# Optimization experiments

Measured on AMD Instinct MI355X. Metric: run time of the kernel, lower is better.

## Reference

```python
import jax, jax.numpy as jnp
import numpy as np

NEG_INF = -1e20


def setup_inputs() -> dict:
    key = jax.random.key(0)
    kq, kk, kv, kl = jax.random.split(key, 4)
    B, NQ, NKV, D_QK, D_V = 16, 2048, 2048, 64, 64
    Q_batch = jax.random.normal(kq, (B, NQ, D_QK), dtype=jnp.float32)
    K_batch = jax.random.normal(kk, (B, NKV, D_QK), dtype=jnp.float32)
    V_batch = jax.random.normal(kv, (B, NKV, D_V), dtype=jnp.float32)
    valid_lens = jax.random.randint(kl, (B,), 0, NKV, dtype=jnp.int32)
    return {"Q_batch": Q_batch, "K_batch": K_batch, "V_batch": V_batch,
            "valid_lens": valid_lens}


def reference(Q_batch, K_batch, V_batch, valid_lens):
    d = Q_batch.shape[-1]
    # scores: (B, n_q, n_kv)
    S = jnp.einsum("bqd,bkd->bqk", Q_batch, K_batch) / jnp.sqrt(
        jnp.asarray(d, dtype=Q_batch.dtype))
    n_kv = S.shape[-1]
    # mask kv positions k >= valid_lens[b] (1-D valid_lens broadcast over queries)
    kv_idx = jnp.arange(n_kv)  # (n_kv,)
    mask = kv_idx[None, None, :] < valid_lens[:, None, None]  # (B,1,n_kv)
    S = jnp.where(mask, S, NEG_INF)
    W = jax.nn.softmax(S, axis=-1)
    # dropout rate is 0.0 (eval) -> identity
    return jnp.einsum("bqk,bkv->bqv", W, V_batch)
```

## Files before the change

### kernel.cpp

```cpp
#include <hip/hip_runtime.h>
#include <hip/hip_bf16.h>


typedef __attribute__((ext_vector_type(8))) short short8;
typedef __attribute__((ext_vector_type(4))) float float4v;
typedef __attribute__((ext_vector_type(16))) float f32x16;

#define BATCH 16
#define NQ 2048
#define NKV 2048
#define DH 64
#define KVB 64
#define NTILES (NKV / KVB)
#define TILE_ELEMS (KVB * DH)
#define NEG_INF -1e20f
#define SCALE_LOG2 0.180336880111120f

__device__ __forceinline__ short f2bf(float x) {
    union { float f; unsigned u; } v; v.f = x;
    unsigned r = (v.u + 0x7fffu + ((v.u >> 16) & 1u)) >> 16;
    return (short)r;
}

__device__ __forceinline__ short8 cvt8(float4v a, float4v b) {
    short8 r;
    r[0] = f2bf(a[0]); r[1] = f2bf(a[1]); r[2] = f2bf(a[2]); r[3] = f2bf(a[3]);
    r[4] = f2bf(b[0]); r[5] = f2bf(b[1]); r[6] = f2bf(b[2]); r[7] = f2bf(b[3]);
    return r;
}

__global__ __launch_bounds__(256) void prep_kernel(
    const float* __restrict__ K, const float* __restrict__ V,
    const int* __restrict__ valid_lens,
    short* __restrict__ Kf, short* __restrict__ Vf)
{
    const int b    = blockIdx.x >> 5;
    const int tile = blockIdx.x & 31;
    const int vlen = valid_lens[b];
    const int nkv  = (vlen == 0) ? NKV : vlen;
    if (tile * KVB >= nkv) return;

    const int tid = threadIdx.x;
    const int ln  = tid & 63;
    const int l31 = ln & 31;
    const int hi8 = (ln >> 5) * 8;
    const size_t gbase = ((size_t)b * NKV + (size_t)tile * KVB) * DH;
    short* kt = Kf + (((size_t)b * NTILES + tile) * TILE_ELEMS);
    short* vt = Vf + (((size_t)b * NTILES + tile) * TILE_ELEMS);

#pragma unroll
    for (int s = 0; s < 2; ++s) {
        const int kk = tid >> 6;
        const int kv = s * 32 + l31;
        const int d  = kk * 16 + hi8;
        const float* p = K + gbase + (size_t)kv * DH + d;
        *reinterpret_cast<short8*>(kt + (s * 256 + tid) * 8) =
            cvt8(*reinterpret_cast<const float4v*>(p),
                 *reinterpret_cast<const float4v*>(p + 4));
    }
#pragma unroll
    for (int t = 0; t < 2; ++t) {
        const int ks  = tid >> 6;
        const int d   = t * 32 + l31;
        const int kv0 = ks * 16 + hi8;
        short8 w;
#pragma unroll
        for (int j = 0; j < 8; ++j)
            w[j] = f2bf(V[gbase + (size_t)(kv0 + j) * DH + d]);
        *reinterpret_cast<short8*>(vt + (t * 256 + tid) * 8) = w;
    }
}

__global__ __launch_bounds__(512) void attn_fwd_kernel(
    const float* __restrict__ Q,
    const short* __restrict__ Kf,
    const short* __restrict__ Vf,
    const int* __restrict__ valid_lens,
    float* __restrict__ O)
{
    __shared__ float  mrg[4][2048];
    __shared__ float2 mlb[4][32];

    const int tid  = threadIdx.x;
    const int wave = tid >> 6;
    const int lane = tid & 63;
    const int l31  = lane & 31;
    const int hi   = lane >> 5;
    const int h    = wave >> 2;
    const int qsub = wave & 3;

    const int b  = blockIdx.x & 15;
    const int qt = blockIdx.x >> 4;
    const int qbase = qt * 128 + qsub * 32;

    const int vlen  = valid_lens[b];
    const int nkv   = (vlen == 0) ? NKV : vlen;
    const int tiles = (nkv + KVB - 1) / KVB;
    const int nh = (tiles + 1 - h) >> 1;

    const float* Qb = Q + ((size_t)b * NQ + qbase + l31) * DH;
    short8 qfrag[4];
#pragma unroll
    for (int kk = 0; kk < 4; ++kk) {
        const float* p = Qb + kk * 16 + hi * 8;
        float4v a = *reinterpret_cast<const float4v*>(p);
        float4v c = *reinterpret_cast<const float4v*>(p + 4);
#pragma unroll
        for (int j = 0; j < 4; ++j) { a[j] *= SCALE_LOG2; c[j] *= SCALE_LOG2; }
        qfrag[kk] = cvt8(a, c);
    }

    const short* Kfb = Kf + (size_t)b * NTILES * TILE_ELEMS + lane * 8;
    const short* Vfb = Vf + (size_t)b * NTILES * TILE_ELEMS + lane * 8;

    auto load_k = [&](short8 (&kf)[8], int tile) {
        const short* p = Kfb + (size_t)tile * TILE_ELEMS;
#pragma unroll
        for (int i = 0; i < 8; ++i)
            kf[i] = *reinterpret_cast<const short8*>(p + i * 512);
    };
    auto load_v = [&](short8 (&vf)[8], int tile) {
        const short* p = Vfb + (size_t)tile * TILE_ELEMS;
#pragma unroll
        for (int i = 0; i < 8; ++i)
            vf[i] = *reinterpret_cast<const short8*>(p + i * 512);
    };

    f32x16 acc_o[2];
#pragma unroll
    for (int t = 0; t < 2; ++t)
#pragma unroll
        for (int r = 0; r < 16; ++r) acc_o[t][r] = 0.f;
    float m = -INFINITY, lsum = 0.f;

    short8 kf0[8], kf1[8], vfr[8];

    auto body = [&](short8 (&kc)[8], short8 (&kn)[8], int it) {
        const int tile = 2 * it + h;
        load_v(vfr, tile);

        f32x16 acs[2];
#pragma unroll
        for (int s = 0; s < 2; ++s)
#pragma unroll
            for (int r = 0; r < 16; ++r) acs[s][r] = 0.f;
        __builtin_amdgcn_s_setprio(1);
#pragma unroll
        for (int s = 0; s < 2; ++s)
#pragma unroll
            for (int kk = 0; kk < 4; ++kk)
                acs[s] = __builtin_amdgcn_mfma_f32_32x32x16_bf16(
                    kc[s * 4 + kk], qfrag[kk], acs[s], 0, 0, 0);
        __builtin_amdgcn_s_setprio(0);

        if (it + 1 < nh) load_k(kn, 2 * (it + 1) + h);

        const int kvb0 = tile * KVB + 4 * hi;
#pragma unroll
        for (int s = 0; s < 2; ++s) {
            const int vlim = vlen - (kvb0 + s * 32);
#pragma unroll
            for (int r = 0; r < 16; ++r) {
                const int rc = (r & 3) + 8 * (r >> 2);
                acs[s][r] = (rc < vlim) ? acs[s][r] : NEG_INF;
            }
        }

        float mx[8];
#pragma unroll
        for (int r = 0; r < 8; ++r)
            mx[r] = fmaxf(fmaxf(acs[0][r], acs[0][r + 8]),
                          fmaxf(acs[1][r], acs[1][r + 8]));
#pragma unroll
        for (int d = 4; d; d >>= 1)
#pragma unroll
            for (int r = 0; r < d; ++r) mx[r] = fmaxf(mx[r], mx[r + d]);
        float x = mx[0];
        x = fmaxf(x, __shfl_xor(x, 32, 64));

        float mn = m;
        if (!__all(x <= m + 8.f)) {
            mn = fmaxf(m, x);
            const float alpha = exp2f(m - mn);
            m = mn;
            lsum *= alpha;
#pragma unroll
            for (int r = 0; r < 16; ++r) {
                const int rc = (r & 3) + 8 * (r >> 2);
                const float ar = __shfl(alpha, rc + 4 * hi, 64);
                acc_o[0][r] *= ar;
                acc_o[1][r] *= ar;
            }
        }

#pragma unroll
        for (int s = 0; s < 2; ++s)
#pragma unroll
            for (int r = 0; r < 16; ++r) acs[s][r] = exp2f(acs[s][r] - mn);
        float sm[8];
#pragma unroll
        for (int r = 0; r < 8; ++r)
            sm[r] = (acs[0][r] + acs[0][r + 8]) + (acs[1][r] + acs[1][r + 8]);
#pragma unroll
        for (int d = 4; d; d >>= 1)
#pragma unroll
            for (int r = 0; r < d; ++r) sm[r] += sm[r + d];
        float rs = sm[0];
        rs += __shfl_xor(rs, 32, 64);
        lsum += rs;

        unsigned pk[2][4][2];
#pragma unroll
        for (int s = 0; s < 2; ++s)
#pragma unroll
            for (int be = 0; be < 4; ++be)
#pragma unroll
                for (int c = 0; c < 2; ++c)
                    asm("v_cvt_pk_bf16_f32 %0, %1, %2"
                        : "=v"(pk[s][be][c])
                        : "v"(acs[s][4 * be + 2 * c]),
                          "v"(acs[s][4 * be + 2 * c + 1]));

        __builtin_amdgcn_s_setprio(1);
#pragma unroll
        for (int ks = 0; ks < 4; ++ks) {
            const int s = ks >> 1, g = ks & 1;
            unsigned w0 = pk[s][2 * g][0], w2 = pk[s][2 * g + 1][0];
            unsigned w1 = pk[s][2 * g][1], w3 = pk[s][2 * g + 1][1];
            asm("v_permlane32_swap_b32 %0, %1" : "+v"(w0), "+v"(w2));
            asm("v_permlane32_swap_b32 %0, %1" : "+v"(w1), "+v"(w3));
            union { unsigned u[4]; short8 s8; } pf;
            pf.u[0] = w0; pf.u[1] = w1; pf.u[2] = w2; pf.u[3] = w3;
#pragma unroll
            for (int t = 0; t < 2; ++t)
                acc_o[t] = __builtin_amdgcn_mfma_f32_32x32x16_bf16(
                    pf.s8, vfr[t * 4 + ks], acc_o[t], 0, 0, 0);
        }
        __builtin_amdgcn_s_setprio(0);
    };

    if (nh > 0) load_k(kf0, h);
    int it = 0;
    for (; it + 1 < nh; it += 2) {
        body(kf0, kf1, it);
        body(kf1, kf0, it + 1);
    }
    if (it < nh) body(kf0, kf1, it);

    if (h == 1) {
#pragma unroll
        for (int t = 0; t < 2; ++t)
#pragma unroll
            for (int r = 0; r < 16; ++r)
                mrg[qsub][(t * 16 + r) * 64 + lane] = acc_o[t][r];
        if (lane < 32) mlb[qsub][lane] = float2{m, lsum};
    }
    __syncthreads();
    if (h == 0) {
        const float2 o1 = mlb[qsub][l31];
        const float m1 = o1.x, l1 = o1.y;
        const float M  = (l1 > 0.f) ? fmaxf(m, m1) : m;
        const float w0 = exp2f(m - M);
        const float w1 = (l1 > 0.f) ? exp2f(m1 - M) : 0.f;
        const float L  = lsum * w0 + l1 * w1;
        const float a0 = w0 / L, a1 = w1 / L;
        float* Ob = O + ((size_t)b * NQ + qbase) * DH;
#pragma unroll
        for (int r = 0; r < 16; ++r) {
            const int rc = (r & 3) + 8 * (r >> 2);
            const float a0r = __shfl(a0, rc + 4 * hi, 64);
            const float a1r = __shfl(a1, rc + 4 * hi, 64);
#pragma unroll
            for (int t = 0; t < 2; ++t) {
                const float oh = mrg[qsub][(t * 16 + r) * 64 + lane];
                Ob[(size_t)(rc + 4 * hi) * DH + t * 32 + l31] =
                    acc_o[t][r] * a0r + oh * a1r;
            }
        }
    }
}

extern "C" void kernel_launch(void* const* d_in, const int* in_sizes, int n_in,
                              void* d_out, int out_size, void* d_ws, size_t ws_size,
                              hipStream_t stream) {
    const float* Q = (const float*)d_in[0];
    const float* K = (const float*)d_in[1];
    const float* V = (const float*)d_in[2];
    const int* vl  = (const int*)d_in[3];
    float* Out     = (float*)d_out;

    short* Kws = (short*)d_ws;
    short* Vws = Kws + (size_t)BATCH * NTILES * TILE_ELEMS;

    prep_kernel<<<dim3(BATCH * NTILES), dim3(256), 0, stream>>>(K, V, vl, Kws, Vws);
    attn_fwd_kernel<<<dim3(BATCH * (NQ / 128)), dim3(512), 0, stream>>>(
        Q, Kws, Vws, vl, Out);
}
```

Before: 43.85 us.

## Split KV range four ways per query tile and coalesce V prep transpose

The attention kernel now handles 64 queries per block, with four waves splitting the KV tiles for each 32-query group instead of two. This doubles the grid and gives each wave fewer serial tiles, which matters because valid lengths vary. Partial results from all four waves are merged through padded shared memory into coalesced float4 output stores. The prep kernel now reads V with vectorized row loads before transposing to bf16 fragments, replacing strided scalar loads. Masking is skipped on tiles that are fully valid. The trade-off is more merge work, more shared memory, and Q being loaded and converted for twice as many blocks.

```diff
diff --git a/kernel.cpp b/kernel.cpp
--- a/kernel.cpp
+++ b/kernel.cpp
@@ -3,6 +3,7 @@
 
 
 typedef __attribute__((ext_vector_type(8))) short short8;
+typedef __attribute__((ext_vector_type(4))) short short4v;
 typedef __attribute__((ext_vector_type(4))) float float4v;
 typedef __attribute__((ext_vector_type(16))) float f32x16;
 
@@ -58,16 +59,27 @@
             cvt8(*reinterpret_cast<const float4v*>(p),
                  *reinterpret_cast<const float4v*>(p + 4));
     }
-#pragma unroll
-    for (int t = 0; t < 2; ++t) {
-        const int ks  = tid >> 6;
-        const int d   = t * 32 + l31;
-        const int kv0 = ks * 16 + hi8;
-        short8 w;
-#pragma unroll
-        for (int j = 0; j < 8; ++j)
-            w[j] = f2bf(V[gbase + (size_t)(kv0 + j) * DH + d]);
-        *reinterpret_cast<short8*>(vt + (t * 256 + tid) * 8) = w;
+    {
+        const int kv0 = (tid >> 4) << 2;
+        const int d0  = (tid & 15) << 2;
+        const float* p = V + gbase + (size_t)kv0 * DH + d0;
+        float4v r0 = *reinterpret_cast<const float4v*>(p);
+        float4v r1 = *reinterpret_cast<const float4v*>(p + DH);
+        float4v r2 = *reinterpret_cast<const float4v*>(p + 2 * DH);
+        float4v r3 = *reinterpret_cast<const float4v*>(p + 3 * DH);
+        const int ks  = kv0 >> 4;
+        const int hiv = (kv0 >> 3) & 1;
+        const int j0  = kv0 & 7;
+#pragma unroll
+        for (int k = 0; k < 4; ++k) {
+            const int d    = d0 + k;
+            const int lanev = (d & 31) + 32 * hiv;
+            short4v w;
+            w[0] = f2bf(r0[k]); w[1] = f2bf(r1[k]);
+            w[2] = f2bf(r2[k]); w[3] = f2bf(r3[k]);
+            *reinterpret_cast<short4v*>(
+                vt + (((d >> 5) * 4 + ks) * 64 + lanev) * 8 + j0) = w;
+        }
     }
 }
 
@@ -78,25 +90,25 @@
     const int* __restrict__ valid_lens,
     float* __restrict__ O)
 {
-    __shared__ float  mrg[4][2048];
-    __shared__ float2 mlb[4][32];
+    __shared__ float  mrg[2][4][32][68];
+    __shared__ float2 mlb[2][4][32];
 
     const int tid  = threadIdx.x;
     const int wave = tid >> 6;
     const int lane = tid & 63;
     const int l31  = lane & 31;
     const int hi   = lane >> 5;
-    const int h    = wave >> 2;
-    const int qsub = wave & 3;
+    const int qsub = wave >> 2;
+    const int kvq  = wave & 3;
 
     const int b  = blockIdx.x & 15;
     const int qt = blockIdx.x >> 4;
-    const int qbase = qt * 128 + qsub * 32;
+    const int qbase = qt * 64 + qsub * 32;
 
     const int vlen  = valid_lens[b];
     const int nkv   = (vlen == 0) ? NKV : vlen;
     const int tiles = (nkv + KVB - 1) / KVB;
-    const int nh = (tiles + 1 - h) >> 1;
+    const int nh    = (tiles - kvq + 3) >> 2;
 
     const float* Qb = Q + ((size_t)b * NQ + qbase + l31) * DH;
     short8 qfrag[4];
@@ -136,7 +148,7 @@
     short8 kf0[8], kf1[8], vfr[8];
 
     auto body = [&](short8 (&kc)[8], short8 (&kn)[8], int it) {
-        const int tile = 2 * it + h;
+        const int tile = 4 * it + kvq;
         load_v(vfr, tile);
 
         f32x16 acs[2];
@@ -153,16 +165,18 @@
                     kc[s * 4 + kk], qfrag[kk], acs[s], 0, 0, 0);
         __builtin_amdgcn_s_setprio(0);
 
-        if (it + 1 < nh) load_k(kn, 2 * (it + 1) + h);
-
-        const int kvb0 = tile * KVB + 4 * hi;
-#pragma unroll
-        for (int s = 0; s < 2; ++s) {
-            const int vlim = vlen - (kvb0 + s * 32);
-#pragma unroll
-            for (int r = 0; r < 16; ++r) {
-                const int rc = (r & 3) + 8 * (r >> 2);
-                acs[s][r] = (rc < vlim) ? acs[s][r] : NEG_INF;
+        if (it + 1 < nh) load_k(kn, 4 * (it + 1) + kvq);
+
+        if (vlen < (tile + 1) * KVB) {
+            const int kvb0 = tile * KVB + 4 * hi;
+#pragma unroll
+            for (int s = 0; s < 2; ++s) {
+                const int vlim = vlen - (kvb0 + s * 32);
+#pragma unroll
+                for (int r = 0; r < 16; ++r) {
+                    const int rc = (r & 3) + 8 * (r >> 2);
+                    acs[s][r] = (rc < vlim) ? acs[s][r] : NEG_INF;
+                }
             }
         }
 
@@ -239,7 +253,7 @@
         __builtin_amdgcn_s_setprio(0);
     };
 
-    if (nh > 0) load_k(kf0, h);
+    if (nh > 0) load_k(kf0, kvq);
     int it = 0;
     for (; it + 1 < nh; it += 2) {
         body(kf0, kf1, it);
@@ -247,36 +261,46 @@
     }
     if (it < nh) body(kf0, kf1, it);
 
-    if (h == 1) {
-#pragma unroll
-        for (int t = 0; t < 2; ++t)
-#pragma unroll
-            for (int r = 0; r < 16; ++r)
-                mrg[qsub][(t * 16 + r) * 64 + lane] = acc_o[t][r];
-        if (lane < 32) mlb[qsub][lane] = float2{m, lsum};
-    }
-    __syncthreads();
-    if (h == 0) {
-        const float2 o1 = mlb[qsub][l31];
-        const float m1 = o1.x, l1 = o1.y;
-        const float M  = (l1 > 0.f) ? fmaxf(m, m1) : m;
-        const float w0 = exp2f(m - M);
-        const float w1 = (l1 > 0.f) ? exp2f(m1 - M) : 0.f;
-        const float L  = lsum * w0 + l1 * w1;
-        const float a0 = w0 / L, a1 = w1 / L;
-        float* Ob = O + ((size_t)b * NQ + qbase) * DH;
+#pragma unroll
+    for (int t = 0; t < 2; ++t)
 #pragma unroll
         for (int r = 0; r < 16; ++r) {
             const int rc = (r & 3) + 8 * (r >> 2);
-            const float a0r = __shfl(a0, rc + 4 * hi, 64);
-            const float a1r = __shfl(a1, rc + 4 * hi, 64);
-#pragma unroll
-            for (int t = 0; t < 2; ++t) {
-                const float oh = mrg[qsub][(t * 16 + r) * 64 + lane];
-                Ob[(size_t)(rc + 4 * hi) * DH + t * 32 + l31] =
-                    acc_o[t][r] * a0r + oh * a1r;
-            }
-        }
+            mrg[qsub][kvq][rc + 4 * hi][t * 32 + l31] = acc_o[t][r];
+        }
+    if (lane < 32) mlb[qsub][kvq][l31] = float2{m, lsum};
+    __syncthreads();
+
+    {
+        const int qsubo = wave >> 2;
+        const int qq = (wave & 3) * 8 + (lane >> 3);
+        const int dg = (lane & 7) * 8;
+        float mi[4], li[4];
+#pragma unroll
+        for (int i = 0; i < 4; ++i) {
+            const float2 c = mlb[qsubo][i][qq];
+            mi[i] = c.x; li[i] = c.y;
+        }
+        const float M = fmaxf(fmaxf(mi[0], mi[1]), fmaxf(mi[2], mi[3]));
+        float wgt[4], L = 0.f;
+#pragma unroll
+        for (int i = 0; i < 4; ++i) { wgt[i] = exp2f(mi[i] - M); L += li[i] * wgt[i]; }
+        const float Linv = 1.f / L;
+#pragma unroll
+        for (int i = 0; i < 4; ++i) wgt[i] *= Linv;
+
+        float4v o0 = {0.f, 0.f, 0.f, 0.f}, o1 = {0.f, 0.f, 0.f, 0.f};
+#pragma unroll
+        for (int i = 0; i < 4; ++i) {
+            const float* src = &mrg[qsubo][i][qq][dg];
+            float4v a = *reinterpret_cast<const float4v*>(src);
+            float4v c = *reinterpret_cast<const float4v*>(src + 4);
+#pragma unroll
+            for (int j = 0; j < 4; ++j) { o0[j] += a[j] * wgt[i]; o1[j] += c[j] * wgt[i]; }
+        }
+        float* Ob = O + ((size_t)b * NQ + qt * 64 + qsubo * 32 + qq) * DH + dg;
+        *reinterpret_cast<float4v*>(Ob)     = o0;
+        *reinterpret_cast<float4v*>(Ob + 4) = o1;
     }
 }
 
@@ -293,6 +317,6 @@
     short* Vws = Kws + (size_t)BATCH * NTILES * TILE_ELEMS;
 
     prep_kernel<<<dim3(BATCH * NTILES), dim3(256), 0, stream>>>(K, V, vl, Kws, Vws);
-    attn_fwd_kernel<<<dim3(BATCH * (NQ / 128)), dim3(512), 0, stream>>>(
+    attn_fwd_kernel<<<dim3(BATCH * (NQ / 64)), dim3(512), 0, stream>>>(
         Q, Kws, Vws, vl, Out);
 }
```

Measured after the change: 46.19 us. 5.3% more time.
